# Kernel optimization log

Measured on AMD Instinct MI355X. Metric: run time of the kernel, lower is better.

The kernel has to match this reference:

```python
import jax, jax.numpy as jnp
import numpy as np

NUDGE = 1e-7

def _norm(x):
    # global mean + L2-norm over axes (1,2), per sample (faithful to source)
    size = x.shape[1] * x.shape[2]
    mean = jnp.sum(x, axis=(1, 2), keepdims=True) / size
    xc = x - mean
    l2 = jnp.sqrt(jnp.sum(xc * xc, axis=(1, 2), keepdims=True))
    return xc / (l2 + NUDGE)


def setup_inputs() -> dict:
    key = jax.random.key(0)
    ks = jax.random.split(key, 9)
    B, D, S, F = 8, 512, 4096, 2048
    s = 0.02
    x = jax.random.normal(ks[0], (B, D, S), dtype=jnp.float32)
    Wq = jax.random.normal(ks[1], (D, D), dtype=jnp.float32) * s
    Wk = jax.random.normal(ks[2], (D, D), dtype=jnp.float32) * s
    Wv = jax.random.normal(ks[3], (D, D), dtype=jnp.float32) * s
    Wo = jax.random.normal(ks[4], (D, D), dtype=jnp.float32) * s
    W1 = jax.random.normal(ks[5], (D, F), dtype=jnp.float32) * s
    b1 = jnp.zeros((F,), dtype=jnp.float32)
    W2 = jax.random.normal(ks[6], (F, D), dtype=jnp.float32) * s
    b2 = jnp.zeros((D,), dtype=jnp.float32)
    return {"x": x, "Wq": Wq, "Wk": Wk, "Wv": Wv, "Wo": Wo,
            "W1": W1, "b1": b1, "W2": W2, "b2": b2}


def reference(x, Wq, Wk, Wv, Wo, W1, b1, W2, b2):
    B, D, S = x.shape
    xt = jnp.swapaxes(x, 1, 2)                      # [B,S,D]
    q = xt @ Wq                                     # [B,S,D]
    k = xt @ Wk
    v = xt @ Wv
    scores = jnp.einsum('bsd,btd->bst', q, k) / jnp.sqrt(jnp.float32(D))
    attn = jax.nn.softmax(scores, axis=-1)          # [B,S,S]
    attn_out = jnp.swapaxes((attn @ v) @ Wo, 1, 2)  # [B,D,S]

    post = _norm(x + attn_out)                      # [B,D,S]

    # per-slice feedforward+linear loop == batched matmul over token axis
    pt = jnp.swapaxes(post, 1, 2)                   # [B,S,D]
    h = jax.nn.relu(pt @ W1 + b1) @ W2 + b2         # [B,S,D]
    return _norm(post + jnp.swapaxes(h, 1, 2))
```

## Files before the change

### kernel.cpp

```cpp
#include <hip/hip_runtime.h>


typedef unsigned short u16;
typedef __attribute__((ext_vector_type(4))) float f32x4;
typedef __attribute__((ext_vector_type(8))) short s16x8;

__device__ __forceinline__ float bf2f(u16 u) {
    unsigned int v = ((unsigned int)u) << 16;
    float f;
    __builtin_memcpy(&f, &v, 4);
    return f;
}
__device__ __forceinline__ u16 f2bf(float f) {
    unsigned int v;
    __builtin_memcpy(&v, &f, 4);
    unsigned int r = (v + 0x7fffu + ((v >> 16) & 1u)) >> 16;
    return (u16)r;
}
__device__ __forceinline__ u16 loadbf(const void* p, long long i, int f32) {
    return f32 ? f2bf(((const float*)p)[i]) : ((const u16*)p)[i];
}

#if defined(__has_builtin)
#if __has_builtin(__builtin_amdgcn_global_load_lds)
#define HAS_GLDS 1
#endif
#endif
#ifndef HAS_GLDS
#define HAS_GLDS 0
#endif

#if HAS_GLDS
__device__ __forceinline__ void glds16(const u16* g, u16* l) {
    __builtin_amdgcn_global_load_lds(
        (const __attribute__((address_space(1))) void*)g,
        (__attribute__((address_space(3))) void*)l, 16, 0, 0);
}
#else
__device__ __forceinline__ void glds16(const u16* g, u16* l) {
    *(int4*)l = *(const int4*)g;
}
#endif

struct DetectArgs { const u16* p[9]; int n[9]; };

__global__ __launch_bounds__(256) void detect9(DetectArgs a, int* __restrict__ flags)
{
    const u16* p = a.p[blockIdx.x];
    const int n_u16 = a.n[blockIdx.x];
    int insane = 0;
    for (int i = threadIdx.x; i < n_u16; i += 256) {
        u16 h = p[i];
        int e = (h >> 7) & 0xFF;
        int m = h & 0x7F;
        bool sane = (e >= 96 && e <= 141) || (e == 0 && m == 0);
        insane += sane ? 0 : 1;
    }
#pragma unroll
    for (int off = 32; off > 0; off >>= 1) insane += __shfl_down(insane, off);
    __shared__ int red[4];
    if ((threadIdx.x & 63) == 0) red[threadIdx.x >> 6] = insane;
    __syncthreads();
    if (threadIdx.x == 0)
        flags[blockIdx.x] = (red[0] + red[1] + red[2] + red[3] > n_u16 / 4) ? 1 : 0;
}

#define BM 128
#define BN 128
#define BK 32

template <typename OutT, bool BIAS, bool RELU>
__global__ __launch_bounds__(256) void gemm_bt(
    const u16* __restrict__ A, const u16* __restrict__ Bt, OutT* __restrict__ C,
    const u16* __restrict__ bias, int M, int N, int K,
    int lda, int ldb, int ldc, int wmod,
    long long aZ, long long aW, long long bZ, long long bW, long long cZ,
    int swz)
{
    __shared__ u16 As[2][BM * BK];
    __shared__ u16 Bs[2][BN * BK];

    const int z = blockIdx.z;
    const int g = z / wmod, w = z - g * wmod;
    A  += g * aZ + w * aW;
    Bt += g * bZ + w * bW;
    C  += (long long)z * cZ;

    int bx = blockIdx.x, by = blockIdx.y;
    if (swz) {
        const int gx = gridDim.x;
        int id = by * gx + bx;
        int xcd = id & 7, j = id >> 3;
        bx = j % gx;
        by = (j / gx) * 8 + xcd;
    }

    const int tid = threadIdx.x;
    const int wave = tid >> 6, lane = tid & 63;
    const int wm = wave >> 1, wn = wave & 1;
    const int q = lane >> 4, r = lane & 15;

    const int ar = tid >> 2;
    const int ac = (((tid & 3) ^ ((tid >> 3) & 3)) << 3);
    const int ks = (r >> 1) & 3;

    const u16* Ag = A + (long long)(by * BM + ar) * lda + ac;
    const u16* Bg = Bt + (long long)(bx * BN + ar) * ldb + ac;
    const long long rstepA = 64LL * lda, rstepB = 64LL * ldb;

    f32x4 acc[4][4];
    const f32x4 zero = {0.f, 0.f, 0.f, 0.f};
#pragma unroll
    for (int i = 0; i < 4; ++i)
#pragma unroll
        for (int j = 0; j < 4; ++j) acc[i][j] = zero;

    const int nIter = K / BK;
    glds16(Ag, &As[0][tid * 8]);
    glds16(Ag + rstepA, &As[0][2048 + tid * 8]);
    glds16(Bg, &Bs[0][tid * 8]);
    glds16(Bg + rstepB, &Bs[0][2048 + tid * 8]);
    Ag += BK; Bg += BK;
    __syncthreads();
    for (int it = 0; it < nIter; ++it) {
        const int cur = it & 1, nxt = cur ^ 1;
        if (it + 1 < nIter) {
            glds16(Ag, &As[nxt][tid * 8]);
            glds16(Ag + rstepA, &As[nxt][2048 + tid * 8]);
            glds16(Bg, &Bs[nxt][tid * 8]);
            glds16(Bg + rstepB, &Bs[nxt][2048 + tid * 8]);
            Ag += BK; Bg += BK;
        }
        s16x8 af[4], bf[4];
#pragma unroll
        for (int mi = 0; mi < 4; ++mi)
            af[mi] = *(const s16x8*)(&As[cur][(wm * 64 + mi * 16 + r) * BK + ((q ^ ks) << 3)]);
#pragma unroll
        for (int ni = 0; ni < 4; ++ni)
            bf[ni] = *(const s16x8*)(&Bs[cur][(wn * 64 + ni * 16 + r) * BK + ((q ^ ks) << 3)]);
#pragma unroll
        for (int mi = 0; mi < 4; ++mi)
#pragma unroll
            for (int ni = 0; ni < 4; ++ni)
                acc[mi][ni] = __builtin_amdgcn_mfma_f32_16x16x32_bf16(
                    af[mi], bf[ni], acc[mi][ni], 0, 0, 0);
        __syncthreads();
    }

    const int col0 = bx * BN + wn * 64;
    const int row0 = by * BM + wm * 64;
#pragma unroll
    for (int ni = 0; ni < 4; ++ni) {
        const int colg = col0 + ni * 16 + r;
        float bv = 0.f;
        if constexpr (BIAS) bv = bf2f(bias[colg]);
#pragma unroll
        for (int mi = 0; mi < 4; ++mi) {
#pragma unroll
            for (int rr = 0; rr < 4; ++rr) {
                const int rowg = row0 + mi * 16 + q * 4 + rr;
                float v = acc[mi][ni][rr] + bv;
                if constexpr (RELU) v = fmaxf(v, 0.f);
                if constexpr (sizeof(OutT) == 2)
                    C[(long long)rowg * ldc + colg] = (OutT)f2bf(v);
                else
                    C[(long long)rowg * ldc + colg] = (OutT)v;
            }
        }
    }
}

template <bool DIRECT>
__global__ __launch_bounds__(512, 2) void flash_attn(
    const u16* __restrict__ QKV,
    const u16* __restrict__ Vt,
    u16* __restrict__ O,
    float* __restrict__ Opart,
    float* __restrict__ rsPart,
    int nsplit)
{
    __shared__ u16 Qs[64 * 512];
    __shared__ u16 Ks[2][128 * 128];
    __shared__ u16 Ps[64 * 136];
    __shared__ float rsL[8][64];

    const long long SD = 4096LL * 512;
    int g = blockIdx.z, qb = blockIdx.x;
    if (gridDim.z == 8 && gridDim.y == 1) {
        int id = g * 64 + qb;
        g = id & 7; qb = id >> 3;
    }
    const int sp = blockIdx.y;
    const int q0 = qb * 64;
    const u16* Qg = QKV + ((long long)g * 3 + 0) * SD;
    const u16* Kg = QKV + ((long long)g * 3 + 1) * SD;
    const u16* Vg = Vt + (long long)g * SD;

    const int tid = threadIdx.x;
    const int wave = tid >> 6, lane = tid & 63;
    const int q = lane >> 4, r = lane & 15;
    const int mg = wave >> 2, ng = wave & 3;
    const int dg = wave;

#pragma unroll
    for (int i = 0; i < 8; ++i) {
        int L = i * 512 + tid;
        int row = L >> 6, p = L & 63;
        int l = p ^ (row & 15);
        glds16(Qg + (long long)(q0 + row) * 512 + l * 8, &Qs[L * 8]);
    }

    f32x4 oacc[4][4];
    const f32x4 zero = {0.f, 0.f, 0.f, 0.f};
#pragma unroll
    for (int i = 0; i < 4; ++i)
#pragma unroll
        for (int j = 0; j < 4; ++j) oacc[i][j] = zero;
    float rsum[2][4] = {{0.f, 0.f, 0.f, 0.f}, {0.f, 0.f, 0.f, 0.f}};

    const int span = 4096 / nsplit;
    const int kt0 = sp * span;
    const int ktN = span / 128;
    const float scale = 0.044194173824159216f;

    auto stageK = [&](int ktile, int kc, int buf) {
#pragma unroll
        for (int i = 0; i < 4; ++i) {
            int L = i * 512 + tid;
            int row = L >> 4, p = L & 15;
            int l = p ^ (row & 15);
            glds16(Kg + (long long)(kt0 + ktile * 128 + row) * 512 + kc * 128 + l * 8,
                   &Ks[buf][L * 8]);
        }
    };
    stageK(0, 0, 0);

    for (int kt = 0; kt < ktN; ++kt) {
        f32x4 sacc[2][2];
#pragma unroll
        for (int i = 0; i < 2; ++i)
#pragma unroll
            for (int j = 0; j < 2; ++j) sacc[i][j] = zero;

        for (int kc = 0; kc < 4; ++kc) {
            __syncthreads();
            if (kc < 3) stageK(kt, kc + 1, (kc + 1) & 1);
            const u16* Kb = Ks[kc & 1];
#pragma unroll
            for (int sc = 0; sc < 4; ++sc) {
                s16x8 af[2], bf[2];
#pragma unroll
                for (int mi = 0; mi < 2; ++mi) {
                    int row = (mg * 2 + mi) * 16 + r;
                    int l = kc * 16 + sc * 4 + q;
                    af[mi] = *(const s16x8*)&Qs[row * 512 + ((l ^ r) << 3)];
                }
#pragma unroll
                for (int ni = 0; ni < 2; ++ni) {
                    int row = (ng * 2 + ni) * 16 + r;
                    int l = sc * 4 + q;
                    bf[ni] = *(const s16x8*)&Kb[row * 128 + ((l ^ r) << 3)];
                }
#pragma unroll
                for (int mi = 0; mi < 2; ++mi)
#pragma unroll
                    for (int ni = 0; ni < 2; ++ni)
                        sacc[mi][ni] = __builtin_amdgcn_mfma_f32_16x16x32_bf16(
                            af[mi], bf[ni], sacc[mi][ni], 0, 0, 0);
            }
        }
#pragma unroll
        for (int mi = 0; mi < 2; ++mi) {
#pragma unroll
            for (int ni = 0; ni < 2; ++ni) {
                int col = (ng * 2 + ni) * 16 + r;
#pragma unroll
                for (int rr = 0; rr < 4; ++rr) {
                    int row = (mg * 2 + mi) * 16 + q * 4 + rr;
                    float v = __expf(fminf(sacc[mi][ni][rr] * scale, 30.f));
                    Ps[row * 136 + col] = f2bf(v);
                    rsum[mi][rr] += v;
                }
            }
        }
        __syncthreads();
        if (kt + 1 < ktN) stageK(kt + 1, 0, 0);
        const long long vbase = (long long)(dg * 64 + r) * 4096 + kt0 + kt * 128;
#pragma unroll
        for (int kc = 0; kc < 4; ++kc) {
            s16x8 af[4], bf[4];
#pragma unroll
            for (int mi = 0; mi < 4; ++mi)
                af[mi] = *(const s16x8*)(Vg + vbase + (long long)mi * 16 * 4096
                                         + kc * 32 + q * 8);
#pragma unroll
            for (int ni = 0; ni < 4; ++ni)
                bf[ni] = *(const s16x8*)&Ps[(ni * 16 + r) * 136 + kc * 32 + q * 8];
            __builtin_amdgcn_s_setprio(1);
#pragma unroll
            for (int mi = 0; mi < 4; ++mi)
#pragma unroll
                for (int ni = 0; ni < 4; ++ni)
                    oacc[mi][ni] = __builtin_amdgcn_mfma_f32_16x16x32_bf16(
                        af[mi], bf[ni], oacc[mi][ni], 0, 0, 0);
            __builtin_amdgcn_s_setprio(0);
        }
    }

#pragma unroll
    for (int mi = 0; mi < 2; ++mi)
#pragma unroll
        for (int rr = 0; rr < 4; ++rr) {
            float s = rsum[mi][rr];
#pragma unroll
            for (int m = 1; m < 16; m <<= 1) s += __shfl_xor(s, m);
            rsum[mi][rr] = s;
        }
    if (r == 0) {
#pragma unroll
        for (int mi = 0; mi < 2; ++mi)
#pragma unroll
            for (int rr = 0; rr < 4; ++rr)
                rsL[wave][(mg * 2 + mi) * 16 + q * 4 + rr] = rsum[mi][rr];
    }
    __syncthreads();

    if constexpr (DIRECT) {
        u16* Og = O + (long long)g * SD;
#pragma unroll
        for (int ni = 0; ni < 4; ++ni) {
            int qrow = ni * 16 + r;
            int wb = (qrow >> 5) * 4;
            float rs = rsL[wb][qrow] + rsL[wb + 1][qrow]
                     + rsL[wb + 2][qrow] + rsL[wb + 3][qrow];
            float inv = 1.f / rs;
#pragma unroll
            for (int mi = 0; mi < 4; ++mi) {
                int d = (dg * 4 + mi) * 16 + q * 4;
                ushort4 o4;
                o4.x = f2bf(oacc[mi][ni][0] * inv);
                o4.y = f2bf(oacc[mi][ni][1] * inv);
                o4.z = f2bf(oacc[mi][ni][2] * inv);
                o4.w = f2bf(oacc[mi][ni][3] * inv);
                *(ushort4*)&Og[(long long)(q0 + qrow) * 512 + d] = o4;
            }
        }
    } else {
        const int pb = g * nsplit + sp;
        float* Op = Opart + (long long)pb * SD;
#pragma unroll
        for (int ni = 0; ni < 4; ++ni) {
            int qrow = ni * 16 + r;
#pragma unroll
            for (int mi = 0; mi < 4; ++mi) {
                int d = (dg * 4 + mi) * 16 + q * 4;
                float4 o4;
                o4.x = oacc[mi][ni][0]; o4.y = oacc[mi][ni][1];
                o4.z = oacc[mi][ni][2]; o4.w = oacc[mi][ni][3];
                *(float4*)&Op[(long long)(q0 + qrow) * 512 + d] = o4;
            }
        }
        if (tid < 64) {
            int wb = (tid >> 5) * 4;
            rsPart[(long long)pb * 4096 + q0 + tid] =
                rsL[wb][tid] + rsL[wb + 1][tid] + rsL[wb + 2][tid] + rsL[wb + 3][tid];
        }
    }
}

__global__ __launch_bounds__(256) void reduce_flash(
    const float* __restrict__ Opart, const float* __restrict__ rsPart,
    u16* __restrict__ O, int ns)
{
    const long long SD = 4096LL * 512;
    const int g = blockIdx.y;
    u16* Og = O + (long long)g * SD;
    const int base = blockIdx.x * 2048;
#pragma unroll
    for (int it = 0; it < 8; ++it) {
        int i = base + it * 256 + threadIdx.x;
        int row = i >> 9;
        float s = 0.f, rs = 0.f;
        for (int sp = 0; sp < ns; ++sp) {
            s += Opart[(long long)(g * ns + sp) * SD + i];
            rs += rsPart[(long long)(g * ns + sp) * 4096 + row];
        }
        Og[i] = f2bf(s / rs);
    }
}

__global__ __launch_bounds__(256) void transpose_any(
    const void* __restrict__ in, u16* __restrict__ out, int R, int C,
    long long sIn, long long sOut, const int* __restrict__ flag)
{
    __shared__ u16 tile[32][33];
    const int f32 = *flag;
    const long long ib = (long long)blockIdx.z * sIn;
    u16* ob = out + (long long)blockIdx.z * sOut;
    const int c0 = blockIdx.x * 32, r0 = blockIdx.y * 32;
    const int tx = threadIdx.x, ty = threadIdx.y;
#pragma unroll
    for (int i = 0; i < 4; ++i) {
        int rr = ty + i * 8;
        tile[rr][tx] = loadbf(in, ib + (long long)(r0 + rr) * C + c0 + tx, f32);
    }
    __syncthreads();
#pragma unroll
    for (int i = 0; i < 4; ++i) {
        int cc = ty + i * 8;
        ob[(long long)(c0 + cc) * R + r0 + tx] = tile[tx][cc];
    }
}

__global__ __launch_bounds__(256) void transpose_b16(
    const u16* __restrict__ in, u16* __restrict__ out, int R, int C,
    long long sIn, long long sOut)
{
    __shared__ u16 tile[32][33];
    in += (long long)blockIdx.z * sIn;
    out += (long long)blockIdx.z * sOut;
    const int c0 = blockIdx.x * 32, r0 = blockIdx.y * 32;
    const int tx = threadIdx.x, ty = threadIdx.y;
#pragma unroll
    for (int i = 0; i < 4; ++i) {
        int rr = ty + i * 8;
        tile[rr][tx] = in[(long long)(r0 + rr) * C + c0 + tx];
    }
    __syncthreads();
#pragma unroll
    for (int i = 0; i < 4; ++i) {
        int cc = ty + i * 8;
        out[(long long)(c0 + cc) * R + r0 + tx] = tile[tx][cc];
    }
}

__global__ __launch_bounds__(256) void convert_bias(
    const void* __restrict__ b1, const void* __restrict__ b2,
    u16* __restrict__ ob, const int* __restrict__ f1, const int* __restrict__ f2)
{
    int i = blockIdx.x * 256 + threadIdx.x;
    if (i < 2048) ob[i] = loadbf(b1, i, *f1);
    else if (i < 2560) ob[i] = loadbf(b2, i - 2048, *f2);
}

__global__ __launch_bounds__(256) void stats_add_partial(
    const u16* __restrict__ A, const u16* __restrict__ Bv,
    float2* __restrict__ partial)
{
    const int b = blockIdx.y;
    const long long yb = (long long)b * (4096LL * 512);
    const int base = blockIdx.x * 2048;
    float s = 0.f, ss = 0.f;
#pragma unroll
    for (int it = 0; it < 8; ++it) {
        int i = base + it * 256 + threadIdx.x;
        float z = bf2f(A[yb + i]) + bf2f(Bv[yb + i]);
        s += z; ss += z * z;
    }
#pragma unroll
    for (int off = 32; off > 0; off >>= 1) {
        s += __shfl_down(s, off); ss += __shfl_down(ss, off);
    }
    __shared__ float red[8];
    int lane = threadIdx.x & 63, wave = threadIdx.x >> 6;
    if (lane == 0) { red[wave * 2] = s; red[wave * 2 + 1] = ss; }
    __syncthreads();
    if (threadIdx.x == 0) {
        for (int w = 1; w < 4; ++w) { s += red[w * 2]; ss += red[w * 2 + 1]; }
        partial[b * 1024 + blockIdx.x] = make_float2(s, ss);
    }
}

__global__ __launch_bounds__(256) void stats_finish(
    const float2* __restrict__ partial, float2* __restrict__ stats, float N)
{
    const int b = blockIdx.x;
    float s = 0.f, ss = 0.f;
    for (int i = threadIdx.x; i < 1024; i += 256) {
        float2 p = partial[b * 1024 + i];
        s += p.x; ss += p.y;
    }
#pragma unroll
    for (int off = 32; off > 0; off >>= 1) {
        s += __shfl_down(s, off); ss += __shfl_down(ss, off);
    }
    __shared__ float red[8];
    int lane = threadIdx.x & 63, wave = threadIdx.x >> 6;
    if (lane == 0) { red[wave * 2] = s; red[wave * 2 + 1] = ss; }
    __syncthreads();
    if (threadIdx.x == 0) {
        for (int w = 1; w < 4; ++w) { s += red[w * 2]; ss += red[w * 2 + 1]; }
        float mean = s / N;
        float l2 = sqrtf(fmaxf(ss - s * s / N, 0.f));
        stats[b] = make_float2(mean, 1.f / (l2 + 1e-7f));
    }
}

__global__ __launch_bounds__(256) void post_kernel(
    const u16* __restrict__ A, const u16* __restrict__ Bv,
    const float2* __restrict__ stats, u16* __restrict__ post)
{
    const int b = blockIdx.y;
    const float2 st = stats[b];
    const long long yb = (long long)b * (4096LL * 512);
    const int base = blockIdx.x * 2048;
#pragma unroll
    for (int it = 0; it < 8; ++it) {
        int i = base + it * 256 + threadIdx.x;
        float z = bf2f(A[yb + i]) + bf2f(Bv[yb + i]);
        post[yb + i] = f2bf((z - st.x) * st.y);
    }
}

__global__ __launch_bounds__(256) void final_kernel(
    const u16* __restrict__ P, const u16* __restrict__ G,
    const float2* __restrict__ stats, float* __restrict__ out)
{
    __shared__ float tile[32][33];
    const int b = blockIdx.z;
    const float2 st = stats[b];
    const long long bb = (long long)b * (4096LL * 512);
    const int s0 = blockIdx.x * 32, d0 = blockIdx.y * 32;
    const int tx = threadIdx.x, ty = threadIdx.y;
#pragma unroll
    for (int i = 0; i < 4; ++i) {
        int sl = ty + i * 8;
        long long idx = bb + (long long)(s0 + sl) * 512 + d0 + tx;
        tile[sl][tx] = bf2f(P[idx]) + bf2f(G[idx]);
    }
    __syncthreads();
#pragma unroll
    for (int i = 0; i < 4; ++i) {
        int dl = ty + i * 8;
        out[bb + (long long)(d0 + dl) * 4096 + s0 + tx] =
            (tile[tx][dl] - st.x) * st.y;
    }
}

extern "C" void kernel_launch(void* const* d_in, const int* in_sizes, int n_in,
                              void* d_out, int out_size, void* d_ws, size_t ws_size,
                              hipStream_t stream)
{
    (void)out_size;
    const void* x  = d_in[0];
    const void* Wq = d_in[1];
    const void* Wk = d_in[2];
    const void* Wv = d_in[3];
    const void* Wo = d_in[4];
    const void* W1 = d_in[5];
    const void* b1 = d_in[6];
    const void* W2 = d_in[7];
    const void* b2 = d_in[8];

    const int Bb = 8, D = 512, S = 4096, F = 2048;
    const long long SD = (long long)S * D;
    const long long DD = (long long)D * D;

    char* ws = (char*)d_ws;
    size_t off = 0;
    auto take = [&](size_t bytes) -> char* {
        char* p = ws + off;
        off += (bytes + 255) & ~(size_t)255;
        return p;
    };
    u16* xt   = (u16*)take((size_t)Bb * SD * 2);
    u16* WqT  = (u16*)take((size_t)DD * 2);
    u16* WkT  = (u16*)take((size_t)DD * 2);
    u16* WvT  = (u16*)take((size_t)DD * 2);
    u16* WoT  = (u16*)take((size_t)DD * 2);
    u16* W1T  = (u16*)take((size_t)D * F * 2);
    u16* W2T  = (u16*)take((size_t)D * F * 2);
    u16* bb   = (u16*)take(2560 * 2);
    u16* post = (u16*)take((size_t)Bb * SD * 2);
    float2* npart  = (float2*)take(8 * 1024 * sizeof(float2));
    float2* stats1v = (float2*)take(256);
    float2* stats2v = (float2*)take(256);
    int* flags = (int*)take(16 * sizeof(int));
    float* rsPart = (float*)take(4 * 4096 * sizeof(float));

    size_t remaining = ws_size > off ? ws_size - off : 0;
    const size_t perG = (size_t)4 * SD * 2 + 4096;
    int G = (remaining >= 8 * perG) ? 8 : (remaining >= 4 * perG) ? 4 : 2;
    int ns = (G >= 4) ? 1 : 2;

    u16* attnBuf = (u16*)take((size_t)4 * G * SD * 2);
    u16* QKVb = attnBuf;
    u16* Vtb  = attnBuf + (size_t)3 * G * SD;
    float* Opart = (float*)post;
    u16* Oall = (u16*)d_out;
    u16* Y    = post;
    u16* Hbuf = (u16*)d_out;
    u16* Gbuf = attnBuf;

    DetectArgs da;
    for (int i = 0; i < 9; ++i) {
        da.p[i] = (const u16*)d_in[i];
        da.n[i] = (i < n_in && in_sizes[i] < 8192) ? in_sizes[i] : 8192;
    }
    detect9<<<dim3(9), 256, 0, stream>>>(da, flags);

    dim3 tb(32, 8, 1);
    transpose_any<<<dim3(S / 32, D / 32, Bb), tb, 0, stream>>>(x, xt, D, S, SD, SD, flags + 0);
    transpose_any<<<dim3(16, 16, 1), tb, 0, stream>>>(Wq, WqT, D, D, 0, 0, flags + 1);
    transpose_any<<<dim3(16, 16, 1), tb, 0, stream>>>(Wk, WkT, D, D, 0, 0, flags + 2);
    transpose_any<<<dim3(16, 16, 1), tb, 0, stream>>>(Wv, WvT, D, D, 0, 0, flags + 3);
    transpose_any<<<dim3(16, 16, 1), tb, 0, stream>>>(Wo, WoT, D, D, 0, 0, flags + 4);
    transpose_any<<<dim3(F / 32, D / 32, 1), tb, 0, stream>>>(W1, W1T, D, F, 0, 0, flags + 5);
    transpose_any<<<dim3(D / 32, F / 32, 1), tb, 0, stream>>>(W2, W2T, F, D, 0, 0, flags + 7);
    convert_bias<<<10, 256, 0, stream>>>(b1, b2, bb, flags + 6, flags + 8);

    for (int b0 = 0; b0 < Bb; b0 += G) {
        gemm_bt<u16, false, false><<<dim3(D / 128, S / 128, 3 * G), 256, 0, stream>>>(
            xt + (long long)b0 * SD, WqT, QKVb, nullptr, S, D, D, D, D, D,
            3, SD, 0, 0, DD, SD, 1);
        transpose_b16<<<dim3(D / 32, S / 32, G), tb, 0, stream>>>(
            QKVb + 2 * SD, Vtb, S, D, 3 * SD, SD);
        if (ns == 1) {
            flash_attn<true><<<dim3(64, 1, G), 512, 0, stream>>>(
                QKVb, Vtb, Oall + (long long)b0 * SD, nullptr, nullptr, 1);
        } else {
            flash_attn<false><<<dim3(64, ns, G), 512, 0, stream>>>(
                QKVb, Vtb, nullptr, Opart, rsPart, ns);
            reduce_flash<<<dim3(1024, G), 256, 0, stream>>>(
                Opart, rsPart, Oall + (long long)b0 * SD, ns);
        }
    }

    gemm_bt<u16, false, false><<<dim3(D / 128, (Bb * S) / 128, 1), 256, 0, stream>>>(
        Oall, WoT, Y, nullptr, Bb * S, D, D, D, D, D, 1, 0, 0, 0, 0, 0, 1);

    stats_add_partial<<<dim3(1024, Bb), 256, 0, stream>>>(xt, Y, npart);
    stats_finish<<<dim3(Bb), 256, 0, stream>>>(npart, stats1v, (float)SD);
    post_kernel<<<dim3(1024, Bb), 256, 0, stream>>>(xt, Y, stats1v, post);

    for (int h = 0; h < 2; ++h) {
        gemm_bt<u16, true, true><<<dim3(F / 128, (4 * S) / 128, 1), 256, 0, stream>>>(
            post + (long long)h * 4 * SD, W1T, Hbuf, bb, 4 * S, F, D, D, D, F,
            1, 0, 0, 0, 0, 0, 1);
        gemm_bt<u16, true, false><<<dim3(D / 128, (4 * S) / 128, 1), 256, 0, stream>>>(
            Hbuf, W2T, Gbuf + (long long)h * 4 * SD, bb + 2048, 4 * S, D, F, F, F, D,
            1, 0, 0, 0, 0, 0, 1);
    }

    stats_add_partial<<<dim3(1024, Bb), 256, 0, stream>>>(post, Gbuf, npart);
    stats_finish<<<dim3(Bb), 256, 0, stream>>>(npart, stats2v, (float)SD);
    final_kernel<<<dim3(S / 32, D / 32, Bb), tb, 0, stream>>>(
        post, Gbuf, stats2v, (float*)d_out);
}
```

Before: 1.035 ms.

## Double flash-attention workgroup to 1024 threads with 16 waves per tile

The flash attention kernel now runs 16 waves per 64-query tile instead of 8. Each wave computes a 32x16 slice of the score tile and a 32-row slice of the output dimension, which halves the per-wave accumulator registers and the per-thread staging work. The goal is more waves in flight to hide latency from the shared-memory K staging and the global V loads. In exchange, the launch bound is now one block per CU, so more waves meet at each barrier, and the Q fragments are reloaded by more waves.

Result: no change. 1.025 ms (-1.0%).

```diff
diff --git a/kernel.cpp b/kernel.cpp
--- a/kernel.cpp
+++ b/kernel.cpp
@@ -171,7 +171,7 @@
 }
 
 template <bool DIRECT>
-__global__ __launch_bounds__(512, 2) void flash_attn(
+__global__ __launch_bounds__(1024, 1) void flash_attn(
     const u16* __restrict__ QKV,
     const u16* __restrict__ Vt,
     u16* __restrict__ O,
@@ -182,7 +182,7 @@
     __shared__ u16 Qs[64 * 512];
     __shared__ u16 Ks[2][128 * 128];
     __shared__ u16 Ps[64 * 136];
-    __shared__ float rsL[8][64];
+    __shared__ float rsL[16][64];
 
     const long long SD = 4096LL * 512;
     int g = blockIdx.z, qb = blockIdx.x;
@@ -199,21 +199,21 @@
     const int tid = threadIdx.x;
     const int wave = tid >> 6, lane = tid & 63;
     const int q = lane >> 4, r = lane & 15;
-    const int mg = wave >> 2, ng = wave & 3;
+    const int mg = wave >> 3, ng = wave & 7;
     const int dg = wave;
 
 #pragma unroll
-    for (int i = 0; i < 8; ++i) {
-        int L = i * 512 + tid;
+    for (int i = 0; i < 4; ++i) {
+        int L = i * 1024 + tid;
         int row = L >> 6, p = L & 63;
         int l = p ^ (row & 15);
         glds16(Qg + (long long)(q0 + row) * 512 + l * 8, &Qs[L * 8]);
     }
 
-    f32x4 oacc[4][4];
+    f32x4 oacc[2][4];
     const f32x4 zero = {0.f, 0.f, 0.f, 0.f};
 #pragma unroll
-    for (int i = 0; i < 4; ++i)
+    for (int i = 0; i < 2; ++i)
 #pragma unroll
         for (int j = 0; j < 4; ++j) oacc[i][j] = zero;
     float rsum[2][4] = {{0.f, 0.f, 0.f, 0.f}, {0.f, 0.f, 0.f, 0.f}};
@@ -225,8 +225,8 @@
 
     auto stageK = [&](int ktile, int kc, int buf) {
 #pragma unroll
-        for (int i = 0; i < 4; ++i) {
-            int L = i * 512 + tid;
+        for (int i = 0; i < 2; ++i) {
+            int L = i * 1024 + tid;
             int row = L >> 4, p = L & 15;
             int l = p ^ (row & 15);
             glds16(Kg + (long long)(kt0 + ktile * 128 + row) * 512 + kc * 128 + l * 8,
@@ -236,48 +236,36 @@
     stageK(0, 0, 0);
 
     for (int kt = 0; kt < ktN; ++kt) {
-        f32x4 sacc[2][2];
-#pragma unroll
-        for (int i = 0; i < 2; ++i)
-#pragma unroll
-            for (int j = 0; j < 2; ++j) sacc[i][j] = zero;
+        f32x4 sacc[2];
+        sacc[0] = zero; sacc[1] = zero;
 
         for (int kc = 0; kc < 4; ++kc) {
             __syncthreads();
             if (kc < 3) stageK(kt, kc + 1, (kc + 1) & 1);
             const u16* Kb = Ks[kc & 1];
+            const int krow = ng * 16 + r;
 #pragma unroll
             for (int sc = 0; sc < 4; ++sc) {
-                s16x8 af[2], bf[2];
+                int lk = sc * 4 + q;
+                s16x8 bf = *(const s16x8*)&Kb[krow * 128 + ((lk ^ r) << 3)];
 #pragma unroll
                 for (int mi = 0; mi < 2; ++mi) {
-                    int row = (mg * 2 + mi) * 16 + r;
+                    int row = mg * 32 + mi * 16 + r;
                     int l = kc * 16 + sc * 4 + q;
-                    af[mi] = *(const s16x8*)&Qs[row * 512 + ((l ^ r) << 3)];
+                    s16x8 af = *(const s16x8*)&Qs[row * 512 + ((l ^ r) << 3)];
+                    sacc[mi] = __builtin_amdgcn_mfma_f32_16x16x32_bf16(
+                        af, bf, sacc[mi], 0, 0, 0);
                 }
-#pragma unroll
-                for (int ni = 0; ni < 2; ++ni) {
-                    int row = (ng * 2 + ni) * 16 + r;
-                    int l = sc * 4 + q;
-                    bf[ni] = *(const s16x8*)&Kb[row * 128 + ((l ^ r) << 3)];
-                }
-#pragma unroll
-                for (int mi = 0; mi < 2; ++mi)
-#pragma unroll
-                    for (int ni = 0; ni < 2; ++ni)
-                        sacc[mi][ni] = __builtin_amdgcn_mfma_f32_16x16x32_bf16(
-                            af[mi], bf[ni], sacc[mi][ni], 0, 0, 0);
             }
         }
-#pragma unroll
-        for (int mi = 0; mi < 2; ++mi) {
-#pragma unroll
-            for (int ni = 0; ni < 2; ++ni) {
-                int col = (ng * 2 + ni) * 16 + r;
+        {
+            int col = ng * 16 + r;
+#pragma unroll
+            for (int mi = 0; mi < 2; ++mi) {
 #pragma unroll
                 for (int rr = 0; rr < 4; ++rr) {
-                    int row = (mg * 2 + mi) * 16 + q * 4 + rr;
-                    float v = __expf(fminf(sacc[mi][ni][rr] * scale, 30.f));
+                    int row = mg * 32 + mi * 16 + q * 4 + rr;
+                    float v = __expf(fminf(sacc[mi][rr] * scale, 30.f));
                     Ps[row * 136 + col] = f2bf(v);
                     rsum[mi][rr] += v;
                 }
@@ -285,12 +273,12 @@
         }
         __syncthreads();
         if (kt + 1 < ktN) stageK(kt + 1, 0, 0);
-        const long long vbase = (long long)(dg * 64 + r) * 4096 + kt0 + kt * 128;
+        const long long vbase = (long long)(dg * 32 + r) * 4096 + kt0 + kt * 128;
 #pragma unroll
         for (int kc = 0; kc < 4; ++kc) {
-            s16x8 af[4], bf[4];
-#pragma unroll
-            for (int mi = 0; mi < 4; ++mi)
+            s16x8 af[2], bf[4];
+#pragma unroll
+            for (int mi = 0; mi < 2; ++mi)
                 af[mi] = *(const s16x8*)(Vg + vbase + (long long)mi * 16 * 4096
                                          + kc * 32 + q * 8);
 #pragma unroll
@@ -298,7 +286,7 @@
                 bf[ni] = *(const s16x8*)&Ps[(ni * 16 + r) * 136 + kc * 32 + q * 8];
             __builtin_amdgcn_s_setprio(1);
 #pragma unroll
-            for (int mi = 0; mi < 4; ++mi)
+            for (int mi = 0; mi < 2; ++mi)
 #pragma unroll
                 for (int ni = 0; ni < 4; ++ni)
                     oacc[mi][ni] = __builtin_amdgcn_mfma_f32_16x16x32_bf16(
@@ -321,7 +309,7 @@
         for (int mi = 0; mi < 2; ++mi)
 #pragma unroll
             for (int rr = 0; rr < 4; ++rr)
-                rsL[wave][(mg * 2 + mi) * 16 + q * 4 + rr] = rsum[mi][rr];
+                rsL[wave][mg * 32 + mi * 16 + q * 4 + rr] = rsum[mi][rr];
     }
     __syncthreads();
 
@@ -330,13 +318,14 @@
 #pragma unroll
         for (int ni = 0; ni < 4; ++ni) {
             int qrow = ni * 16 + r;
-            int wb = (qrow >> 5) * 4;
-            float rs = rsL[wb][qrow] + rsL[wb + 1][qrow]
-                     + rsL[wb + 2][qrow] + rsL[wb + 3][qrow];
+            int wb = (qrow >> 5) * 8;
+            float rs = 0.f;
+#pragma unroll
+            for (int j = 0; j < 8; ++j) rs += rsL[wb + j][qrow];
             float inv = 1.f / rs;
 #pragma unroll
-            for (int mi = 0; mi < 4; ++mi) {
-                int d = (dg * 4 + mi) * 16 + q * 4;
+            for (int mi = 0; mi < 2; ++mi) {
+                int d = dg * 32 + mi * 16 + q * 4;
                 ushort4 o4;
                 o4.x = f2bf(oacc[mi][ni][0] * inv);
                 o4.y = f2bf(oacc[mi][ni][1] * inv);
@@ -352,8 +341,8 @@
         for (int ni = 0; ni < 4; ++ni) {
             int qrow = ni * 16 + r;
 #pragma unroll
-            for (int mi = 0; mi < 4; ++mi) {
-                int d = (dg * 4 + mi) * 16 + q * 4;
+            for (int mi = 0; mi < 2; ++mi) {
+                int d = dg * 32 + mi * 16 + q * 4;
                 float4 o4;
                 o4.x = oacc[mi][ni][0]; o4.y = oacc[mi][ni][1];
                 o4.z = oacc[mi][ni][2]; o4.w = oacc[mi][ni][3];
@@ -361,9 +350,11 @@
             }
         }
         if (tid < 64) {
-            int wb = (tid >> 5) * 4;
-            rsPart[(long long)pb * 4096 + q0 + tid] =
-                rsL[wb][tid] + rsL[wb + 1][tid] + rsL[wb + 2][tid] + rsL[wb + 3][tid];
+            int wb = (tid >> 5) * 8;
+            float rs = 0.f;
+#pragma unroll
+            for (int j = 0; j < 8; ++j) rs += rsL[wb + j][tid];
+            rsPart[(long long)pb * 4096 + q0 + tid] = rs;
         }
     }
 }
@@ -616,10 +607,10 @@
         transpose_b16<<<dim3(D / 32, S / 32, G), tb, 0, stream>>>(
             QKVb + 2 * SD, Vtb, S, D, 3 * SD, SD);
         if (ns == 1) {
-            flash_attn<true><<<dim3(64, 1, G), 512, 0, stream>>>(
+            flash_attn<true><<<dim3(64, 1, G), 1024, 0, stream>>>(
                 QKVb, Vtb, Oall + (long long)b0 * SD, nullptr, nullptr, 1);
         } else {
-            flash_attn<false><<<dim3(64, ns, G), 512, 0, stream>>>(
+            flash_attn<false><<<dim3(64, ns, G), 1024, 0, stream>>>(
                 QKVb, Vtb, nullptr, Opart, rsPart, ns);
             reduce_flash<<<dim3(1024, G), 256, 0, stream>>>(
                 Opart, rsPart, Oall + (long long)b0 * SD, ns);
```
